# Kernel tuning notes

Measured on AMD Instinct MI355X. Metric: run time of the kernel, lower is better.

The kernel has to match this reference:

```python
import jax, jax.numpy as jnp
import numpy as np


def _chamfer(pred, target):
    # pred: [B, N, 3], target: [B, M, 3]
    # Squared euclidean pairwise distances (norm=2 in pytorch3d semantics):
    # d[b,n,m] = |p|^2 + |t|^2 - 2 p.t
    p2 = jnp.sum(pred * pred, axis=-1)      # [B, N]
    t2 = jnp.sum(target * target, axis=-1)  # [B, M]
    pt = jnp.einsum('bnd,bmd->bnm', pred, target)  # [B, N, M]
    d = p2[:, :, None] + t2[:, None, :] - 2.0 * pt  # [B, N, M]
    # bidirectional nearest-neighbor min-reduction
    cham_x = jnp.min(d, axis=2)  # [B, N] pred -> target
    cham_y = jnp.min(d, axis=1)  # [B, M] target -> pred
    # point_reduction='mean' then batch_reduction='mean' (pytorch3d defaults)
    loss = jnp.mean(jnp.mean(cham_x, axis=1) + jnp.mean(cham_y, axis=1))
    return loss


def setup_inputs() -> dict:
    key = jax.random.key(0)
    k1, k2 = jax.random.split(key)
    B, N, M, D = 16, 4096, 4096, 3
    pred = jax.random.normal(k1, (B, N, D), dtype=jnp.float32)
    target = jax.random.normal(k2, (B, M, D), dtype=jnp.float32)
    return {"pred": pred, "target": target}


def reference(pred, target):
    return _chamfer(pred, target)
```

## Files before the change

### kernel.cpp

```cpp
#include <hip/hip_runtime.h>

typedef __attribute__((ext_vector_type(8)))  short short8;
typedef __attribute__((ext_vector_type(16))) float f32x16;

#define B_SZ  16
#define NPTS  4096
#define MBLK  512
#define PRB   256
#define NCH   (NPTS / PRB)
#define STGT  1024
#define STILE (STGT / 32)
#define NSTG  (NPTS / STGT)
#define PPT   (STGT / MBLK)
#define NRT   (B_SZ * NPTS)

__device__ __forceinline__ unsigned short f2bf(float f) {
    unsigned u = __float_as_uint(f);
    return (unsigned short)((u + 0x7FFFu + ((u >> 16) & 1u)) >> 16);
}
__device__ __forceinline__ float bf2f(unsigned short s) {
    return __uint_as_float(((unsigned)s) << 16);
}
__device__ __forceinline__ short n2(unsigned short s) {
    return (short)f2bf(-2.0f * bf2f(s));
}

__global__ __launch_bounds__(MBLK, 2) void chamfer_fused(
    const float* __restrict__ pred, const float* __restrict__ target,
    float* __restrict__ out)
{
    __shared__ short8   sB[STILE * 64];
    __shared__ unsigned rowOut[PRB];
    __shared__ float    red[MBLK / 64];

    const int dir = blockIdx.y;
    const float* own = dir ? target : pred;
    const float* opp = dir ? pred : target;

    const int b     = blockIdx.x >> 4;
    const int chunk = blockIdx.x & (NCH - 1);
    const int tid   = threadIdx.x;
    const int lane  = tid & 63;
    const int w     = tid >> 6;
    const int r32   = lane & 31;
    const int h     = lane >> 5;
    const short ONE = (short)0x3F80;

    short8 af;
    {
        const float* pp = own +
            ((size_t)b*NPTS + chunk*PRB + w*32 + r32)*3;
        float x = pp[0], y = pp[1], z = pp[2];
        unsigned short phx=f2bf(x), phy=f2bf(y), phz=f2bf(z);
        unsigned short plx=f2bf(x-bf2f(phx)), ply=f2bf(y-bf2f(phy)),
                       plz=f2bf(z-bf2f(phz));
        short8 v;
        if (h == 0) {
            v[0]=n2(phx); v[1]=n2(phy); v[2]=n2(phz);
            v[3]=n2(plx); v[4]=n2(ply); v[5]=n2(plz);
            v[6]=n2(phx); v[7]=n2(phy);
        } else {
            float p2 = fmaf(z,z,fmaf(y,y,x*x));
            unsigned short p2h=f2bf(p2), p2l=f2bf(p2-bf2f(p2h));
            v[0]=n2(phz); v[1]=n2(plx); v[2]=n2(ply); v[3]=n2(plz);
            v[4]=(short)p2h; v[5]=(short)p2l; v[6]=ONE; v[7]=ONE;
        }
        af = v;
    }

    f32x16 zc;
    #pragma unroll
    for (int r = 0; r < 16; ++r) zc[r] = 0.0f;
    short8 mA = {0,0,0,0,0,0,0,0}, mB = {0,0,0,0,0,0,0,0};
    if (h == 0) { mA[0] = (short)f2bf((float)r32); mB[0] = ONE; }
    f32x16 pr = __builtin_amdgcn_mfma_f32_32x32x16_bf16(mA, mB, zc, 0, 0, 0);
    int lab[16];
    bool ok = true;
    #pragma unroll
    for (int r = 0; r < 16; ++r) {
        lab[r] = ((int)(pr[r] + 0.5f)) & 31;
        ok = ok && (lab[r] == ((r & 3) + 8 * (r >> 2) + 4 * h));
    }
    const bool fast = __all(ok) != 0;

    if (!fast) rowOut[tid & (PRB - 1)] = 0x7F7F7F7Fu;

    f32x16 rmin;
    #pragma unroll
    for (int r = 0; r < 16; ++r) rmin[r] = 1e30f;

    const float* oppB = opp + (size_t)b * NPTS * 3;

    float rx[PPT], ry[PPT], rz[PPT];
    #pragma unroll
    for (int j = 0; j < PPT; ++j) {
        const float* o = oppB + (size_t)(j * MBLK + tid) * 3;
        rx[j] = o[0]; ry[j] = o[1]; rz[j] = o[2];
    }

    for (int s = 0; s < NSTG; ++s) {
        __syncthreads();
        #pragma unroll
        for (int j = 0; j < PPT; ++j) {
            int p  = j * MBLK + tid;
            int t  = p >> 5, cc = p & 31;
            float tx = rx[j], ty = ry[j], tz = rz[j];
            unsigned short hx=f2bf(tx), hy=f2bf(ty), hz=f2bf(tz);
            unsigned short lx=f2bf(tx-bf2f(hx)), ly=f2bf(ty-bf2f(hy)),
                           lz=f2bf(tz-bf2f(hz));
            float t2 = fmaf(tz,tz,fmaf(ty,ty,tx*tx));
            unsigned short t2h=f2bf(t2), t2l=f2bf(t2-bf2f(t2h));
            short8 v0, v1;
            v0[0]=(short)hx; v0[1]=(short)hy; v0[2]=(short)hz;
            v0[3]=(short)hx; v0[4]=(short)hy; v0[5]=(short)hz;
            v0[6]=(short)lx; v0[7]=(short)ly;
            v1[0]=(short)lz; v1[1]=(short)lx; v1[2]=(short)ly;
            v1[3]=(short)lz; v1[4]=ONE; v1[5]=ONE;
            v1[6]=(short)t2h; v1[7]=(short)t2l;
            sB[t*64 + cc]      = v0;
            sB[t*64 + 32 + cc] = v1;
        }
        __syncthreads();

        if (s + 1 < NSTG) {
            #pragma unroll
            for (int j = 0; j < PPT; ++j) {
                const float* o = oppB +
                    (size_t)((s + 1) * STGT + j * MBLK + tid) * 3;
                rx[j] = o[0]; ry[j] = o[1]; rz[j] = o[2];
            }
        }

        for (int t = 0; t < STILE; ++t) {
            short8 b0 = sB[t*64 + lane];
            f32x16 a0 = __builtin_amdgcn_mfma_f32_32x32x16_bf16(af, b0, zc, 0,0,0);
            #pragma unroll
            for (int r = 0; r < 16; ++r)
                rmin[r] = fminf(a0[r], rmin[r]);
        }
    }

    __syncthreads();
    if (fast) {
        #pragma unroll
        for (int r = 0; r < 16; ++r) {
            float v0 = rmin[r];
            v0 = fminf(v0, __shfl_xor(v0, 1, 64));
            v0 = fminf(v0, __shfl_xor(v0, 2, 64));
            v0 = fminf(v0, __shfl_xor(v0, 4, 64));
            v0 = fminf(v0, __shfl_xor(v0, 8, 64));
            v0 = fminf(v0, __shfl_xor(v0, 16, 64));
            if (r32 == 0)
                rowOut[w*32 + lab[r]] = __float_as_uint(v0);
        }
    } else {
        #pragma unroll
        for (int r = 0; r < 16; ++r)
            atomicMin(&rowOut[w*32 + lab[r]],
                      __float_as_uint(fmaxf(rmin[r], 0.0f)));
    }
    __syncthreads();

    float v = (tid < PRB) ? __uint_as_float(rowOut[tid]) : 0.0f;
    for (int off = 32; off > 0; off >>= 1)
        v += __shfl_down(v, off, 64);
    if ((tid & 63) == 0) red[w] = v;
    __syncthreads();
    if (tid == 0) {
        float s = 0.0f;
        #pragma unroll
        for (int i = 0; i < MBLK / 64; ++i) s += red[i];
        atomicAdd(out, s * (1.0f / (float)NRT));
    }
}

extern "C" void kernel_launch(void* const* d_in, const int* in_sizes, int n_in,
                              void* d_out, int out_size, void* d_ws, size_t ws_size,
                              hipStream_t stream) {
    const float* pred   = (const float*)d_in[0];
    const float* target = (const float*)d_in[1];
    float* out = (float*)d_out;

    hipMemsetAsync(out, 0, sizeof(float), stream);

    dim3 grid(B_SZ * NCH, 2);
    chamfer_fused<<<grid, MBLK, 0, stream>>>(pred, target, out);
}
```

Baseline: 33.78 us.

## Process two row fragments per wave to reuse each LDS B-tile

```diff
diff --git a/kernel.cpp b/kernel.cpp
--- a/kernel.cpp
+++ b/kernel.cpp
@@ -5,7 +5,8 @@
 
 #define B_SZ  16
 #define NPTS  4096
-#define MBLK  512
+#define MBLK  256
+#define NFR   2
 #define PRB   256
 #define NCH   (NPTS / PRB)
 #define STGT  1024
@@ -46,10 +47,11 @@
     const int h     = lane >> 5;
     const short ONE = (short)0x3F80;
 
-    short8 af;
-    {
+    short8 af[NFR];
+    #pragma unroll
+    for (int f = 0; f < NFR; ++f) {
         const float* pp = own +
-            ((size_t)b*NPTS + chunk*PRB + w*32 + r32)*3;
+            ((size_t)b*NPTS + chunk*PRB + w*64 + f*32 + r32)*3;
         float x = pp[0], y = pp[1], z = pp[2];
         unsigned short phx=f2bf(x), phy=f2bf(y), phz=f2bf(z);
         unsigned short plx=f2bf(x-bf2f(phx)), ply=f2bf(y-bf2f(phy)),
@@ -65,7 +67,7 @@
             v[0]=n2(phz); v[1]=n2(plx); v[2]=n2(ply); v[3]=n2(plz);
             v[4]=(short)p2h; v[5]=(short)p2l; v[6]=ONE; v[7]=ONE;
         }
-        af = v;
+        af[f] = v;
     }
 
     f32x16 zc;
@@ -83,11 +85,11 @@
     }
     const bool fast = __all(ok) != 0;
 
-    if (!fast) rowOut[tid & (PRB - 1)] = 0x7F7F7F7Fu;
-
-    f32x16 rmin;
-    #pragma unroll
-    for (int r = 0; r < 16; ++r) rmin[r] = 1e30f;
+    if (!fast) rowOut[tid] = 0x7F7F7F7Fu;
+
+    f32x16 rmin0, rmin1;
+    #pragma unroll
+    for (int r = 0; r < 16; ++r) { rmin0[r] = 1e30f; rmin1[r] = 1e30f; }
 
     const float* oppB = opp + (size_t)b * NPTS * 3;
 
@@ -133,10 +135,13 @@
 
         for (int t = 0; t < STILE; ++t) {
             short8 b0 = sB[t*64 + lane];
-            f32x16 a0 = __builtin_amdgcn_mfma_f32_32x32x16_bf16(af, b0, zc, 0,0,0);
+            f32x16 a0 = __builtin_amdgcn_mfma_f32_32x32x16_bf16(af[0], b0, zc, 0,0,0);
+            f32x16 a1 = __builtin_amdgcn_mfma_f32_32x32x16_bf16(af[1], b0, zc, 0,0,0);
             #pragma unroll
-            for (int r = 0; r < 16; ++r)
-                rmin[r] = fminf(a0[r], rmin[r]);
+            for (int r = 0; r < 16; ++r) {
+                rmin0[r] = fminf(a0[r], rmin0[r]);
+                rmin1[r] = fminf(a1[r], rmin1[r]);
+            }
         }
     }
 
@@ -144,24 +149,35 @@
     if (fast) {
         #pragma unroll
         for (int r = 0; r < 16; ++r) {
-            float v0 = rmin[r];
+            float v0 = rmin0[r];
             v0 = fminf(v0, __shfl_xor(v0, 1, 64));
             v0 = fminf(v0, __shfl_xor(v0, 2, 64));
             v0 = fminf(v0, __shfl_xor(v0, 4, 64));
             v0 = fminf(v0, __shfl_xor(v0, 8, 64));
             v0 = fminf(v0, __shfl_xor(v0, 16, 64));
-            if (r32 == 0)
-                rowOut[w*32 + lab[r]] = __float_as_uint(v0);
+            float v1 = rmin1[r];
+            v1 = fminf(v1, __shfl_xor(v1, 1, 64));
+            v1 = fminf(v1, __shfl_xor(v1, 2, 64));
+            v1 = fminf(v1, __shfl_xor(v1, 4, 64));
+            v1 = fminf(v1, __shfl_xor(v1, 8, 64));
+            v1 = fminf(v1, __shfl_xor(v1, 16, 64));
+            if (r32 == 0) {
+                rowOut[w*64 +  0 + lab[r]] = __float_as_uint(v0);
+                rowOut[w*64 + 32 + lab[r]] = __float_as_uint(v1);
+            }
         }
     } else {
         #pragma unroll
-        for (int r = 0; r < 16; ++r)
-            atomicMin(&rowOut[w*32 + lab[r]],
-                      __float_as_uint(fmaxf(rmin[r], 0.0f)));
+        for (int r = 0; r < 16; ++r) {
+            atomicMin(&rowOut[w*64 +  0 + lab[r]],
+                      __float_as_uint(fmaxf(rmin0[r], 0.0f)));
+            atomicMin(&rowOut[w*64 + 32 + lab[r]],
+                      __float_as_uint(fmaxf(rmin1[r], 0.0f)));
+        }
     }
     __syncthreads();
 
-    float v = (tid < PRB) ? __uint_as_float(rowOut[tid]) : 0.0f;
+    float v = __uint_as_float(rowOut[tid]);
     for (int off = 32; off > 0; off >>= 1)
         v += __shfl_down(v, off, 64);
     if ((tid & 63) == 0) red[w] = v;
```

After: 35.52 us. 1.05x slower.
